# Kernel optimization log

Measured on AMD Instinct MI355X. Metric: run time of the kernel, lower is better.

## Reference

```python
import jax, jax.numpy as jnp
import numpy as np

N = 50000
E = 600000
LLM_DIM = 640
HIDDEN = 128
STRUCT_DIM = 16
N_STRUCT_TYPES = 5
N_LAYERS = 2
LN_EPS = 1e-5


def setup_inputs() -> dict:
    key = jax.random.key(0)
    ks = jax.random.split(key, 10)
    llm_feat = jax.random.normal(ks[0], (N, LLM_DIM), dtype=jnp.float32)
    struct_type_ids = jax.random.randint(ks[1], (N,), 0, N_STRUCT_TYPES, dtype=jnp.int64)
    edge_index = jax.random.randint(ks[2], (2, E), 0, N, dtype=jnp.int64)
    proj_out = HIDDEN - STRUCT_DIM  # 112
    proj_W = jax.random.normal(ks[3], (LLM_DIM, proj_out), dtype=jnp.float32) / np.sqrt(LLM_DIM)
    proj_b = jnp.zeros((proj_out,), dtype=jnp.float32)
    struct_emb = jax.random.normal(ks[4], (N_STRUCT_TYPES, STRUCT_DIM), dtype=jnp.float32)
    gcn_W = jax.random.normal(ks[5], (N_LAYERS, HIDDEN, HIDDEN), dtype=jnp.float32) / np.sqrt(HIDDEN)
    gcn_b = jnp.zeros((N_LAYERS, HIDDEN), dtype=jnp.float32)
    ln_g = jnp.ones((HIDDEN,), dtype=jnp.float32)
    ln_b = jnp.zeros((HIDDEN,), dtype=jnp.float32)
    return dict(llm_feat=llm_feat, struct_type_ids=struct_type_ids, edge_index=edge_index,
                proj_W=proj_W, proj_b=proj_b, struct_emb=struct_emb,
                gcn_W=gcn_W, gcn_b=gcn_b, ln_g=ln_g, ln_b=ln_b)


def _gcn_conv(x, src, dst, deg_inv_sqrt, W, b):
    """PyG GCNConv: x' = D^{-1/2}(A+I)D^{-1/2} (x W) + b, D over A+I."""
    xw = x @ W  # [N, H]
    norm = deg_inv_sqrt[src] * deg_inv_sqrt[dst]  # [E]
    msg = xw[src] * norm[:, None]  # [E, H]
    agg = jax.ops.segment_sum(msg, dst, num_segments=N)  # [N, H]
    # self-loop contribution: norm_ii = deg_i^{-1}
    agg = agg + xw * (deg_inv_sqrt * deg_inv_sqrt)[:, None]
    return agg + b


def reference(llm_feat, struct_type_ids, edge_index, proj_W, proj_b,
              struct_emb, gcn_W, gcn_b, ln_g, ln_b):
    x_llm = llm_feat @ proj_W + proj_b  # [N, hidden-struct_dim]
    x_struct = struct_emb[struct_type_ids]  # [N, struct_dim]
    x = jnp.concatenate([x_llm, x_struct], axis=-1)  # [N, hidden]

    src, dst = edge_index[0], edge_index[1]
    # degree with self-loops (A + I)
    deg = 1.0 + jax.ops.segment_sum(jnp.ones((E,), dtype=x.dtype), dst, num_segments=N)
    deg_inv_sqrt = jax.lax.rsqrt(deg)

    for l in range(N_LAYERS):
        x_new = jax.nn.relu(_gcn_conv(x, src, dst, deg_inv_sqrt, gcn_W[l], gcn_b[l]))
        # dropout is identity in eval mode
        x = x + x_new

    mean = jnp.mean(x, axis=-1, keepdims=True)
    var = jnp.mean(jnp.square(x - mean), axis=-1, keepdims=True)
    return (x - mean) * jax.lax.rsqrt(var + LN_EPS) * ln_g + ln_b
```

## Files before the change

kernel.cpp:

```cpp
#include <hip/hip_runtime.h>

#define N_NODES 50000
#define E_EDGES 600000
#define LLM_DIM 640
#define HIDDEN 128
#define POUT 112
#define NB_SCAN 98

typedef __attribute__((ext_vector_type(8))) short bf16x8;
typedef __attribute__((ext_vector_type(4))) float f32x4;

__device__ inline unsigned short f2bf(float f) {
    unsigned u = __float_as_uint(f);
    u += 0x7fff + ((u >> 16) & 1);
    return (unsigned short)(u >> 16);
}
__device__ inline float bflo(unsigned v) { return __uint_as_float(v << 16); }
__device__ inline float bfhi(unsigned v) { return __uint_as_float(v & 0xffff0000u); }

__global__ void deg_count(const int* __restrict__ eidx, int* __restrict__ cnt) {
    int e = blockIdx.x * 256 + threadIdx.x;
    if (e < E_EDGES) atomicAdd(&cnt[eidx[E_EDGES + e]], 1);
}

__global__ void make_dis(const int* __restrict__ cnt, float* __restrict__ dis) {
    int i = blockIdx.x * 256 + threadIdx.x;
    if (i < N_NODES) dis[i] = rsqrtf(1.0f + (float)cnt[i]);
}

__global__ __launch_bounds__(256) void scan_blocksum(const int* __restrict__ cnt, int* __restrict__ bsum) {
    __shared__ int s[256];
    int b = blockIdx.x, t = threadIdx.x;
    int i0 = b * 512 + t, i1 = i0 + 256;
    int v = (i0 < N_NODES ? cnt[i0] : 0) + (i1 < N_NODES ? cnt[i1] : 0);
    s[t] = v;
    __syncthreads();
    for (int st = 128; st; st >>= 1) {
        if (t < st) s[t] += s[t + st];
        __syncthreads();
    }
    if (t == 0) bsum[b] = s[0];
}

__global__ void scan_bsum(const int* __restrict__ bsum, int* __restrict__ bpre) {
    __shared__ int s[128];
    int t = threadIdx.x;
    if (t < NB_SCAN) s[t] = bsum[t];
    __syncthreads();
    if (t == 0) {
        int a = 0;
        for (int i = 0; i < NB_SCAN; i++) { int v = s[i]; s[i] = a; a += v; }
    }
    __syncthreads();
    if (t < NB_SCAN) bpre[t] = s[t];
}

__global__ __launch_bounds__(256) void scan_offs(const int* __restrict__ cnt, const int* __restrict__ bpre,
                                                 int* __restrict__ offs) {
    __shared__ int sA[512], sB[512];
    int b = blockIdx.x, t = threadIdx.x;
    int i0 = b * 512 + t, i1 = i0 + 256;
    int v0 = (i0 < N_NODES ? cnt[i0] : 0);
    int v1 = (i1 < N_NODES ? cnt[i1] : 0);
    sA[t] = v0; sA[t + 256] = v1;
    int* src = sA; int* dst = sB;
    for (int st = 1; st < 512; st <<= 1) {
        __syncthreads();
        dst[t]       = src[t]       + (t       >= st ? src[t - st]       : 0);
        dst[t + 256] = src[t + 256] + (t + 256 >= st ? src[t + 256 - st] : 0);
        int* tmp = src; src = dst; dst = tmp;
    }
    __syncthreads();
    int base = bpre[b];
    if (i0 < N_NODES) offs[i0] = base + src[t] - v0;
    if (i1 < N_NODES) offs[i1] = base + src[t + 256] - v1;
    if (b == 0 && t == 0) offs[N_NODES] = E_EDGES;
}

__global__ void fill_srcs(const int* __restrict__ eidx, const int* __restrict__ offs,
                          int* __restrict__ pos, int* __restrict__ srcs) {
    int e = blockIdx.x * 256 + threadIdx.x;
    if (e >= E_EDGES) return;
    int s = eidx[e];
    int d = eidx[E_EDGES + e];
    int p = atomicAdd(&pos[d], 1);
    srcs[offs[d] + p] = s;
}

__global__ void wt_convert(const float* __restrict__ W, unsigned short* __restrict__ Wt) {
    int idx = blockIdx.x * 256 + threadIdx.x;
    if (idx >= POUT * LLM_DIM) return;
    int n = idx / LLM_DIM;
    int k = idx - n * LLM_DIM;
    Wt[(size_t)n * LLM_DIM + k] = f2bf(W[(size_t)k * POUT + n]);
}

__global__ void w2_convert(const float* __restrict__ W, unsigned short* __restrict__ Wt2) {
    int idx = blockIdx.x * 256 + threadIdx.x;
    if (idx >= 2 * HIDDEN * HIDDEN) return;
    int l = idx >> 14;
    int rem = idx & 16383;
    int n = rem >> 7;
    int k = rem & 127;
    Wt2[idx] = f2bf(W[l * 16384 + k * 128 + n]);
}

__global__ __launch_bounds__(256) void proj_mfma(const float* __restrict__ A,
                                                 const unsigned short* __restrict__ Wt,
                                                 const float* __restrict__ bias,
                                                 const float* __restrict__ emb,
                                                 const int* __restrict__ sid,
                                                 const float* __restrict__ dis,
                                                 float* __restrict__ X,
                                                 unsigned short* __restrict__ Xs) {
    const int tid = threadIdx.x;
    const int wave = tid >> 6, lane = tid & 63;
    const int l15 = lane & 15, l4 = lane >> 4;
    const int row0 = blockIdx.x * 64;

    int arow = row0 + wave * 16 + l15;
    if (arow >= N_NODES) arow = N_NODES - 1;
    const float* Ap = A + (size_t)arow * LLM_DIM + l4 * 8;
    const unsigned short* Bp = Wt + (size_t)l15 * LLM_DIM + l4 * 8;

    f32x4 acc[7];
#pragma unroll
    for (int j = 0; j < 7; j++) acc[j] = (f32x4){0.f, 0.f, 0.f, 0.f};

    float4 a[2][2];
    a[0][0] = *reinterpret_cast<const float4*>(Ap);
    a[0][1] = *reinterpret_cast<const float4*>(Ap + 4);

#pragma unroll
    for (int t = 0; t < 20; t++) {
        const int cur = t & 1, nxt = cur ^ 1;
        if (t < 19) {
            const int k1 = (t + 1) * 32;
            a[nxt][0] = *reinterpret_cast<const float4*>(Ap + k1);
            a[nxt][1] = *reinterpret_cast<const float4*>(Ap + k1 + 4);
        }
        bf16x8 b[7];
        const int k0 = t * 32;
#pragma unroll
        for (int ct = 0; ct < 7; ct++)
            b[ct] = *reinterpret_cast<const bf16x8*>(Bp + (size_t)ct * 16 * LLM_DIM + k0);
        bf16x8 av;
        unsigned* ap = reinterpret_cast<unsigned*>(&av);
        ap[0] = (unsigned)f2bf(a[cur][0].x) | ((unsigned)f2bf(a[cur][0].y) << 16);
        ap[1] = (unsigned)f2bf(a[cur][0].z) | ((unsigned)f2bf(a[cur][0].w) << 16);
        ap[2] = (unsigned)f2bf(a[cur][1].x) | ((unsigned)f2bf(a[cur][1].y) << 16);
        ap[3] = (unsigned)f2bf(a[cur][1].z) | ((unsigned)f2bf(a[cur][1].w) << 16);
#pragma unroll
        for (int ct = 0; ct < 7; ct++)
            acc[ct] = __builtin_amdgcn_mfma_f32_16x16x32_bf16(av, b[ct], acc[ct], 0, 0, 0);
    }

#pragma unroll
    for (int r = 0; r < 4; r++) {
        int row = row0 + wave * 16 + l4 * 4 + r;
        if (row >= N_NODES) continue;
        float d = dis[row];
#pragma unroll
        for (int ct = 0; ct < 7; ct++) {
            int col = ct * 16 + l15;
            float v = acc[ct][r] + bias[col];
            X[(size_t)row * HIDDEN + col] = v;
            Xs[(size_t)row * HIDDEN + col] = f2bf(d * v);
        }
        float e = emb[sid[row] * 16 + l15];
        X[(size_t)row * HIDDEN + POUT + l15] = e;
        Xs[(size_t)row * HIDDEN + POUT + l15] = f2bf(d * e);
    }
}

__global__ __launch_bounds__(256) void gather(const unsigned short* __restrict__ Xs,
                                              const int* __restrict__ offs,
                                              const int* __restrict__ srcs,
                                              const float* __restrict__ dis,
                                              unsigned short* __restrict__ Gb) {
    int node = blockIdx.x * 4 + (threadIdx.x >> 6);
    int lane = threadIdx.x & 63;
    if (node >= N_NODES) return;
    int beg = __builtin_amdgcn_readfirstlane(offs[node]);
    int end = __builtin_amdgcn_readfirstlane(offs[node + 1]);
    const unsigned* X32 = reinterpret_cast<const unsigned*>(Xs);
    float ax = 0.f, ay = 0.f;
    int e = beg;
    while (e < end) {
        int n = end - e;
        if (n > 64) n = 64;
        int idx = (lane < n) ? srcs[e + lane] : 0;
        int j = 0;
        for (; j + 4 <= n; j += 4) {
            int s0 = __shfl(idx, j);
            int s1 = __shfl(idx, j + 1);
            int s2 = __shfl(idx, j + 2);
            int s3 = __shfl(idx, j + 3);
            unsigned v0 = X32[(size_t)s0 * 64 + lane];
            unsigned v1 = X32[(size_t)s1 * 64 + lane];
            unsigned v2 = X32[(size_t)s2 * 64 + lane];
            unsigned v3 = X32[(size_t)s3 * 64 + lane];
            ax += (bflo(v0) + bflo(v1)) + (bflo(v2) + bflo(v3));
            ay += (bfhi(v0) + bfhi(v1)) + (bfhi(v2) + bfhi(v3));
        }
        for (; j < n; j++) {
            int s = __shfl(idx, j);
            unsigned v = X32[(size_t)s * 64 + lane];
            ax += bflo(v);
            ay += bfhi(v);
        }
        e += 64;
    }
    float d = dis[node];
    unsigned sv = X32[(size_t)node * 64 + lane];
    ax = d * (ax + bflo(sv));
    ay = d * (ay + bfhi(sv));
    reinterpret_cast<unsigned*>(Gb)[(size_t)node * 64 + lane] =
        (unsigned)f2bf(ax) | ((unsigned)f2bf(ay) << 16);
}

template <int MODE>
__global__ __launch_bounds__(256) void gemm_fin(const unsigned short* __restrict__ Gb,
                                                const unsigned short* __restrict__ Wt2,
                                                const float* __restrict__ bias,
                                                const float* __restrict__ dis,
                                                const float* __restrict__ lng,
                                                const float* __restrict__ lnb,
                                                float* __restrict__ X,
                                                unsigned short* __restrict__ Xs2) {
    __shared__ short As[64][136];
    __shared__ short Bs[128][136];
    const int tid = threadIdx.x;
    const int wave = tid >> 6, lane = tid & 63;
    const int row0 = blockIdx.x * 64;
    const int l15 = lane & 15, l4 = lane >> 4;

#pragma unroll
    for (int i = 0; i < 4; i++) {
        int f = i * 256 + tid;
        int r = f >> 4;
        int q = f & 15;
        int grow = row0 + r;
        uint4 v = make_uint4(0, 0, 0, 0);
        if (grow < N_NODES)
            v = reinterpret_cast<const uint4*>(Gb + (size_t)grow * HIDDEN)[q];
        *reinterpret_cast<uint4*>(&As[r][q * 8]) = v;
    }
#pragma unroll
    for (int i = 0; i < 8; i++) {
        int f = i * 256 + tid;
        int r = f >> 4;
        int q = f & 15;
        uint4 v = reinterpret_cast<const uint4*>(Wt2 + (size_t)r * HIDDEN)[q];
        *reinterpret_cast<uint4*>(&Bs[r][q * 8]) = v;
    }
    __syncthreads();

    f32x4 acc[8];
#pragma unroll
    for (int j = 0; j < 8; j++) acc[j] = (f32x4){0.f, 0.f, 0.f, 0.f};
#pragma unroll
    for (int ks = 0; ks < 4; ks++) {
        int kk = ks * 32 + l4 * 8;
        bf16x8 a = *reinterpret_cast<bf16x8*>(&As[wave * 16 + l15][kk]);
#pragma unroll
        for (int ct = 0; ct < 8; ct++) {
            bf16x8 b = *reinterpret_cast<bf16x8*>(&Bs[ct * 16 + l15][kk]);
            acc[ct] = __builtin_amdgcn_mfma_f32_16x16x32_bf16(a, b, acc[ct], 0, 0, 0);
        }
    }

    float bcol[8];
#pragma unroll
    for (int ct = 0; ct < 8; ct++) bcol[ct] = bias[ct * 16 + l15];

    float vv[8][4];
#pragma unroll
    for (int r = 0; r < 4; r++) {
        int row = row0 + wave * 16 + l4 * 4 + r;
        bool ok = row < N_NODES;
#pragma unroll
        for (int ct = 0; ct < 8; ct++) {
            float xo = ok ? X[(size_t)row * HIDDEN + ct * 16 + l15] : 0.f;
            vv[ct][r] = xo + fmaxf(acc[ct][r] + bcol[ct], 0.f);
        }
    }

    if (MODE == 0) {
#pragma unroll
        for (int r = 0; r < 4; r++) {
            int row = row0 + wave * 16 + l4 * 4 + r;
            if (row >= N_NODES) continue;
            float d = dis[row];
#pragma unroll
            for (int ct = 0; ct < 8; ct++) {
                int col = ct * 16 + l15;
                X[(size_t)row * HIDDEN + col] = vv[ct][r];
                Xs2[(size_t)row * HIDDEN + col] = f2bf(d * vv[ct][r]);
            }
        }
    } else {
        float s[4], q2[4];
#pragma unroll
        for (int r = 0; r < 4; r++) {
            s[r] = 0.f; q2[r] = 0.f;
#pragma unroll
            for (int ct = 0; ct < 8; ct++) {
                s[r] += vv[ct][r];
                q2[r] += vv[ct][r] * vv[ct][r];
            }
        }
#pragma unroll
        for (int off = 1; off < 16; off <<= 1) {
#pragma unroll
            for (int r = 0; r < 4; r++) {
                s[r] += __shfl_xor(s[r], off);
                q2[r] += __shfl_xor(q2[r], off);
            }
        }
        float gcol[8], bcol2[8];
#pragma unroll
        for (int ct = 0; ct < 8; ct++) {
            gcol[ct] = lng[ct * 16 + l15];
            bcol2[ct] = lnb[ct * 16 + l15];
        }
#pragma unroll
        for (int r = 0; r < 4; r++) {
            int row = row0 + wave * 16 + l4 * 4 + r;
            if (row >= N_NODES) continue;
            float mean = s[r] * (1.f / 128.f);
            float var = q2[r] * (1.f / 128.f) - mean * mean;
            float inv = rsqrtf(var + 1e-5f);
#pragma unroll
            for (int ct = 0; ct < 8; ct++) {
                int col = ct * 16 + l15;
                X[(size_t)row * HIDDEN + col] = (vv[ct][r] - mean) * inv * gcol[ct] + bcol2[ct];
            }
        }
    }
}

extern "C" void kernel_launch(void* const* d_in, const int* in_sizes, int n_in,
                              void* d_out, int out_size, void* d_ws, size_t ws_size,
                              hipStream_t stream) {
    const float* llm   = (const float*)d_in[0];
    const int*   sid   = (const int*)d_in[1];
    const int*   eidx  = (const int*)d_in[2];
    const float* projW = (const float*)d_in[3];
    const float* projb = (const float*)d_in[4];
    const float* emb   = (const float*)d_in[5];
    const float* gcnW  = (const float*)d_in[6];
    const float* gcnb  = (const float*)d_in[7];
    const float* lng   = (const float*)d_in[8];
    const float* lnb   = (const float*)d_in[9];

    float* X = (float*)d_out;
    unsigned short* Xs = (unsigned short*)d_ws;
    unsigned short* Gb = Xs + (size_t)N_NODES * HIDDEN;
    unsigned short* Wt = Gb;
    unsigned short* Wt2 = Gb + (size_t)N_NODES * HIDDEN;
    float* dis = (float*)(Wt2 + 2 * HIDDEN * HIDDEN);
    int* cnt  = (int*)(dis + N_NODES);
    int* offs = cnt + N_NODES;
    int* bsum = offs + N_NODES + 1;
    int* bpre = bsum + 128;
    int* srcs = bpre + 128;

    hipMemsetAsync(cnt, 0, N_NODES * sizeof(int), stream);
    deg_count<<<(E_EDGES + 255) / 256, 256, 0, stream>>>(eidx, cnt);
    make_dis<<<(N_NODES + 255) / 256, 256, 0, stream>>>(cnt, dis);
    scan_blocksum<<<NB_SCAN, 256, 0, stream>>>(cnt, bsum);
    scan_bsum<<<1, 128, 0, stream>>>(bsum, bpre);
    scan_offs<<<NB_SCAN, 256, 0, stream>>>(cnt, bpre, offs);
    hipMemsetAsync(cnt, 0, N_NODES * sizeof(int), stream);
    fill_srcs<<<(E_EDGES + 255) / 256, 256, 0, stream>>>(eidx, offs, cnt, srcs);

    wt_convert<<<(POUT * LLM_DIM + 255) / 256, 256, 0, stream>>>(projW, Wt);
    w2_convert<<<(2 * HIDDEN * HIDDEN + 255) / 256, 256, 0, stream>>>(gcnW, Wt2);

    proj_mfma<<<(N_NODES + 63) / 64, 256, 0, stream>>>(llm, Wt, projb, emb, sid, dis, X, Xs);

    gather<<<(N_NODES + 3) / 4, 256, 0, stream>>>(Xs, offs, srcs, dis, Gb);
    gemm_fin<0><<<(N_NODES + 63) / 64, 256, 0, stream>>>(Gb, Wt2, gcnb, dis, lng, lnb, X, Xs);
    gather<<<(N_NODES + 3) / 4, 256, 0, stream>>>(Xs, offs, srcs, dis, Gb);
    gemm_fin<1><<<(N_NODES + 63) / 64, 256, 0, stream>>>(Gb, Wt2 + HIDDEN * HIDDEN, gcnb + HIDDEN, dis, lng, lnb, X, Xs);
}
```

Baseline: 434.5 us.

## Stage projection GEMM A tiles through LDS with direct global-to-LDS loads

The projection GEMM kernel now copies 64x32 fp32 tiles of the LLM features into a double-buffered, XOR-swizzled LDS buffer using global_load_lds, instead of each lane issuing strided float4 global loads. The weight fragments are also double-buffered in registers, and the K loop is no longer unrolled. The aim is coalesced, asynchronous streaming of the large A matrix to improve bandwidth on this memory-bound GEMM. In exchange it adds block-wide barriers on every K step, 16KB of LDS per block, and reliance on the swizzle and the builtin's semantics being correct.

```diff
diff --git a/kernel.cpp b/kernel.cpp
--- a/kernel.cpp
+++ b/kernel.cpp
@@ -17,6 +17,12 @@
 }
 __device__ inline float bflo(unsigned v) { return __uint_as_float(v << 16); }
 __device__ inline float bfhi(unsigned v) { return __uint_as_float(v & 0xffff0000u); }
+
+__device__ inline void glds16(const void* g, void* l) {
+    __builtin_amdgcn_global_load_lds(
+        (const __attribute__((address_space(1))) unsigned*)g,
+        (__attribute__((address_space(3))) unsigned*)l, 16, 0, 0);
+}
 
 __global__ void deg_count(const int* __restrict__ eidx, int* __restrict__ cnt) {
     int e = blockIdx.x * 256 + threadIdx.x;
@@ -113,46 +119,90 @@
                                                  const float* __restrict__ dis,
                                                  float* __restrict__ X,
                                                  unsigned short* __restrict__ Xs) {
-    const int tid = threadIdx.x;
+    __shared__ __align__(16) float Ab[2][64 * 32];
+    const int tid  = threadIdx.x;
     const int wave = tid >> 6, lane = tid & 63;
     const int l15 = lane & 15, l4 = lane >> 4;
     const int row0 = blockIdx.x * 64;
 
-    int arow = row0 + wave * 16 + l15;
-    if (arow >= N_NODES) arow = N_NODES - 1;
-    const float* Ap = A + (size_t)arow * LLM_DIM + l4 * 8;
+    const int sr = wave * 8 + (lane >> 3);
+    const int sp = lane & 7;
+    const int sc = (sp ^ (sr & 7)) << 2;
+    int gr0 = row0 + sr;      if (gr0 > N_NODES - 1) gr0 = N_NODES - 1;
+    int gr1 = row0 + 32 + sr; if (gr1 > N_NODES - 1) gr1 = N_NODES - 1;
+    const float* sa0 = A + (size_t)gr0 * LLM_DIM + sc;
+    const float* sa1 = A + (size_t)gr1 * LLM_DIM + sc;
+    const int d0 = wave * 256;
+    const int d1 = 1024 + wave * 256;
+
+    const int rr = wave * 16 + l15;
+    const int ps0 = ((l4 << 1)    ) ^ (l15 & 7);
+    const int ps1 = ((l4 << 1) | 1) ^ (l15 & 7);
+    const int ra0 = rr * 32 + ps0 * 4;
+    const int ra1 = rr * 32 + ps1 * 4;
+
     const unsigned short* Bp = Wt + (size_t)l15 * LLM_DIM + l4 * 8;
 
     f32x4 acc[7];
 #pragma unroll
     for (int j = 0; j < 7; j++) acc[j] = (f32x4){0.f, 0.f, 0.f, 0.f};
 
-    float4 a[2][2];
-    a[0][0] = *reinterpret_cast<const float4*>(Ap);
-    a[0][1] = *reinterpret_cast<const float4*>(Ap + 4);
-
-#pragma unroll
-    for (int t = 0; t < 20; t++) {
-        const int cur = t & 1, nxt = cur ^ 1;
-        if (t < 19) {
-            const int k1 = (t + 1) * 32;
-            a[nxt][0] = *reinterpret_cast<const float4*>(Ap + k1);
-            a[nxt][1] = *reinterpret_cast<const float4*>(Ap + k1 + 4);
-        }
-        bf16x8 b[7];
-        const int k0 = t * 32;
-#pragma unroll
-        for (int ct = 0; ct < 7; ct++)
-            b[ct] = *reinterpret_cast<const bf16x8*>(Bp + (size_t)ct * 16 * LLM_DIM + k0);
-        bf16x8 av;
-        unsigned* ap = reinterpret_cast<unsigned*>(&av);
-        ap[0] = (unsigned)f2bf(a[cur][0].x) | ((unsigned)f2bf(a[cur][0].y) << 16);
-        ap[1] = (unsigned)f2bf(a[cur][0].z) | ((unsigned)f2bf(a[cur][0].w) << 16);
-        ap[2] = (unsigned)f2bf(a[cur][1].x) | ((unsigned)f2bf(a[cur][1].y) << 16);
-        ap[3] = (unsigned)f2bf(a[cur][1].z) | ((unsigned)f2bf(a[cur][1].w) << 16);
-#pragma unroll
-        for (int ct = 0; ct < 7; ct++)
-            acc[ct] = __builtin_amdgcn_mfma_f32_16x16x32_bf16(av, b[ct], acc[ct], 0, 0, 0);
+    glds16(sa0, &Ab[0][d0]);
+    glds16(sa1, &Ab[0][d1]);
+    sa0 += 32; sa1 += 32;
+    bf16x8 bc[7], bn[7];
+#pragma unroll
+    for (int ct = 0; ct < 7; ct++)
+        bc[ct] = *reinterpret_cast<const bf16x8*>(Bp + (size_t)ct * 16 * LLM_DIM);
+    const unsigned short* pb = Bp + 32;
+    __syncthreads();
+
+#pragma unroll 1
+    for (int tt = 0; tt < 10; tt++) {
+        {
+            glds16(sa0, &Ab[1][d0]);
+            glds16(sa1, &Ab[1][d1]);
+            sa0 += 32; sa1 += 32;
+#pragma unroll
+            for (int ct = 0; ct < 7; ct++)
+                bn[ct] = *reinterpret_cast<const bf16x8*>(pb + (size_t)ct * 16 * LLM_DIM);
+            pb += 32;
+            f32x4 va0 = *reinterpret_cast<const f32x4*>(&Ab[0][ra0]);
+            f32x4 va1 = *reinterpret_cast<const f32x4*>(&Ab[0][ra1]);
+            bf16x8 av;
+            unsigned* ap = reinterpret_cast<unsigned*>(&av);
+            ap[0] = (unsigned)f2bf(va0[0]) | ((unsigned)f2bf(va0[1]) << 16);
+            ap[1] = (unsigned)f2bf(va0[2]) | ((unsigned)f2bf(va0[3]) << 16);
+            ap[2] = (unsigned)f2bf(va1[0]) | ((unsigned)f2bf(va1[1]) << 16);
+            ap[3] = (unsigned)f2bf(va1[2]) | ((unsigned)f2bf(va1[3]) << 16);
+#pragma unroll
+            for (int ct = 0; ct < 7; ct++)
+                acc[ct] = __builtin_amdgcn_mfma_f32_16x16x32_bf16(av, bc[ct], acc[ct], 0, 0, 0);
+            __syncthreads();
+        }
+        {
+            if (tt < 9) {
+                glds16(sa0, &Ab[0][d0]);
+                glds16(sa1, &Ab[0][d1]);
+                sa0 += 32; sa1 += 32;
+#pragma unroll
+                for (int ct = 0; ct < 7; ct++)
+                    bc[ct] = *reinterpret_cast<const bf16x8*>(pb + (size_t)ct * 16 * LLM_DIM);
+                pb += 32;
+            }
+            f32x4 va0 = *reinterpret_cast<const f32x4*>(&Ab[1][ra0]);
+            f32x4 va1 = *reinterpret_cast<const f32x4*>(&Ab[1][ra1]);
+            bf16x8 av;
+            unsigned* ap = reinterpret_cast<unsigned*>(&av);
+            ap[0] = (unsigned)f2bf(va0[0]) | ((unsigned)f2bf(va0[1]) << 16);
+            ap[1] = (unsigned)f2bf(va0[2]) | ((unsigned)f2bf(va0[3]) << 16);
+            ap[2] = (unsigned)f2bf(va1[0]) | ((unsigned)f2bf(va1[1]) << 16);
+            ap[3] = (unsigned)f2bf(va1[2]) | ((unsigned)f2bf(va1[3]) << 16);
+#pragma unroll
+            for (int ct = 0; ct < 7; ct++)
+                acc[ct] = __builtin_amdgcn_mfma_f32_16x16x32_bf16(av, bn[ct], acc[ct], 0, 0, 0);
+            if (tt < 9) __syncthreads();
+        }
     }
 
 #pragma unroll
```

Result: faster. 416.9 us (-4.0%).

## Stage projection A tile in swizzled LDS as bf16 with coalesced loads

Applied to the files above, without the earlier changes.

The projection GEMM kernel now loads each block's 64x640 fp32 A tile from global memory with fully coalesced float4 loads, converts it to bf16 once, and stores it into an XOR-swizzled shared-memory buffer. The MFMA loop then reads A fragments from LDS and double-buffers the B (weight) fragments in registers. The aim is to replace the strided per-lane global A reads with contiguous ones and to overlap weight loads with MFMA work. In exchange it uses 80 KB of LDS per block, which limits occupancy, and adds a block-wide barrier before any compute starts.

```diff
diff --git a/kernel.cpp b/kernel.cpp
--- a/kernel.cpp
+++ b/kernel.cpp
@@ -14,6 +14,9 @@
     unsigned u = __float_as_uint(f);
     u += 0x7fff + ((u >> 16) & 1);
     return (unsigned short)(u >> 16);
+}
+__device__ inline unsigned pkbf(float a, float b) {
+    return (unsigned)f2bf(a) | ((unsigned)f2bf(b) << 16);
 }
 __device__ inline float bflo(unsigned v) { return __uint_as_float(v << 16); }
 __device__ inline float bfhi(unsigned v) { return __uint_as_float(v & 0xffff0000u); }
@@ -113,46 +116,80 @@
                                                  const float* __restrict__ dis,
                                                  float* __restrict__ X,
                                                  unsigned short* __restrict__ Xs) {
-    const int tid = threadIdx.x;
+    __shared__ __align__(16) unsigned short As[64 * 640];
+    const int tid  = threadIdx.x;
     const int wave = tid >> 6, lane = tid & 63;
     const int l15 = lane & 15, l4 = lane >> 4;
     const int row0 = blockIdx.x * 64;
 
-    int arow = row0 + wave * 16 + l15;
-    if (arow >= N_NODES) arow = N_NODES - 1;
-    const float* Ap = A + (size_t)arow * LLM_DIM + l4 * 8;
+#pragma unroll
+    for (int half = 0; half < 2; half++) {
+        float4 v[20];
+        int lidx[10];
+#pragma unroll
+        for (int j = 0; j < 10; j++) {
+            int s = (half * 10 + j) * 256 + tid;
+            int row = s / 80;
+            int sl = s - row * 80;
+            int phys = sl ^ (row & 7);
+            lidx[j] = row * 640 + phys * 8;
+            int grow = row0 + row; if (grow >= N_NODES) grow = N_NODES - 1;
+            const float4* gp = reinterpret_cast<const float4*>(A + (size_t)grow * LLM_DIM + sl * 8);
+            v[2 * j]     = gp[0];
+            v[2 * j + 1] = gp[1];
+        }
+#pragma unroll
+        for (int j = 0; j < 10; j++) {
+            uint4 u;
+            u.x = pkbf(v[2 * j].x,     v[2 * j].y);
+            u.y = pkbf(v[2 * j].z,     v[2 * j].w);
+            u.z = pkbf(v[2 * j + 1].x, v[2 * j + 1].y);
+            u.w = pkbf(v[2 * j + 1].z, v[2 * j + 1].w);
+            *reinterpret_cast<uint4*>(&As[lidx[j]]) = u;
+        }
+    }
+
     const unsigned short* Bp = Wt + (size_t)l15 * LLM_DIM + l4 * 8;
+    bf16x8 bc[7], bn[7];
+#pragma unroll
+    for (int ct = 0; ct < 7; ct++)
+        bc[ct] = *reinterpret_cast<const bf16x8*>(Bp + (size_t)ct * 16 * LLM_DIM);
+
+    __syncthreads();
+
+    const int arow = wave * 16 + l15;
+    const int abase = arow * 640;
+    const int rsw = l15 & 7;
 
     f32x4 acc[7];
 #pragma unroll
     for (int j = 0; j < 7; j++) acc[j] = (f32x4){0.f, 0.f, 0.f, 0.f};
 
-    float4 a[2][2];
-    a[0][0] = *reinterpret_cast<const float4*>(Ap);
-    a[0][1] = *reinterpret_cast<const float4*>(Ap + 4);
-
-#pragma unroll
-    for (int t = 0; t < 20; t++) {
-        const int cur = t & 1, nxt = cur ^ 1;
-        if (t < 19) {
-            const int k1 = (t + 1) * 32;
-            a[nxt][0] = *reinterpret_cast<const float4*>(Ap + k1);
-            a[nxt][1] = *reinterpret_cast<const float4*>(Ap + k1 + 4);
-        }
-        bf16x8 b[7];
-        const int k0 = t * 32;
-#pragma unroll
-        for (int ct = 0; ct < 7; ct++)
-            b[ct] = *reinterpret_cast<const bf16x8*>(Bp + (size_t)ct * 16 * LLM_DIM + k0);
-        bf16x8 av;
-        unsigned* ap = reinterpret_cast<unsigned*>(&av);
-        ap[0] = (unsigned)f2bf(a[cur][0].x) | ((unsigned)f2bf(a[cur][0].y) << 16);
-        ap[1] = (unsigned)f2bf(a[cur][0].z) | ((unsigned)f2bf(a[cur][0].w) << 16);
-        ap[2] = (unsigned)f2bf(a[cur][1].x) | ((unsigned)f2bf(a[cur][1].y) << 16);
-        ap[3] = (unsigned)f2bf(a[cur][1].z) | ((unsigned)f2bf(a[cur][1].w) << 16);
-#pragma unroll
-        for (int ct = 0; ct < 7; ct++)
-            acc[ct] = __builtin_amdgcn_mfma_f32_16x16x32_bf16(av, b[ct], acc[ct], 0, 0, 0);
+#pragma unroll
+    for (int ks2 = 0; ks2 < 10; ks2++) {
+        const int ks0 = ks2 * 2;
+        {
+#pragma unroll
+            for (int ct = 0; ct < 7; ct++)
+                bn[ct] = *reinterpret_cast<const bf16x8*>(Bp + (size_t)ct * 16 * LLM_DIM + (ks0 + 1) * 32);
+            int phys = (ks0 * 4 + l4) ^ rsw;
+            bf16x8 a = *reinterpret_cast<const bf16x8*>(&As[abase + phys * 8]);
+#pragma unroll
+            for (int ct = 0; ct < 7; ct++)
+                acc[ct] = __builtin_amdgcn_mfma_f32_16x16x32_bf16(a, bc[ct], acc[ct], 0, 0, 0);
+        }
+        {
+            if (ks2 < 9) {
+#pragma unroll
+                for (int ct = 0; ct < 7; ct++)
+                    bc[ct] = *reinterpret_cast<const bf16x8*>(Bp + (size_t)ct * 16 * LLM_DIM + (ks0 + 2) * 32);
+            }
+            int phys = ((ks0 + 1) * 4 + l4) ^ rsw;
+            bf16x8 a = *reinterpret_cast<const bf16x8*>(&As[abase + phys * 8]);
+#pragma unroll
+            for (int ct = 0; ct < 7; ct++)
+                acc[ct] = __builtin_amdgcn_mfma_f32_16x16x32_bf16(a, bn[ct], acc[ct], 0, 0, 0);
+        }
     }
 
 #pragma unroll
```

New measurement: 438.7 us. Within noise of the previous version (+1.0%).
